# Optimization experiments

Measured on AMD Instinct MI355X. Metric: run time of the kernel, lower is better.

## Reference

```python
import jax, jax.numpy as jnp
import numpy as np

L, D, H, d = 16, 1024, 16, 64
NB, BS = 1024, 16        # num physical blocks, block size (tokens per block)
START_POS = 16368        # T = START_POS + L = 16384
SCALE = 1.0 / np.sqrt(d)


def setup_inputs() -> dict:
    key = jax.random.key(0)
    ks = jax.random.split(key, 5)
    return {
        "x": jax.random.normal(ks[0], (L, D), jnp.float32),
        "k_pool": jax.random.normal(ks[1], (NB, BS, H, d), jnp.float32),
        "v_pool": jax.random.normal(ks[2], (NB, BS, H, d), jnp.float32),
        "W_attn": jax.random.normal(ks[3], (D, 3 * D), jnp.float32) * 0.02,
        "b_attn": jnp.zeros((3 * D,), jnp.float32),
        "W_proj": jax.random.normal(ks[4], (D, D), jnp.float32) * 0.02,
        "b_proj": jnp.zeros((D,), jnp.float32),
        "block_ids": jnp.arange(NB, dtype=jnp.int64),
        "start_pos": START_POS,
    }


def reference(x, k_pool, v_pool, W_attn, b_attn, W_proj, b_proj, block_ids, start_pos):
    # QKV projection
    qkv = x @ W_attn + b_attn                      # [L, 3D]
    q, k, v = jnp.split(qkv, 3, axis=-1)
    q = q.reshape(L, H, d)
    k = k.reshape(L, H, d)
    v = v.reshape(L, H, d)

    # paged write of new K/V into the pool
    pos = start_pos + jnp.arange(L)                # logical positions of new tokens
    blk = block_ids[pos // BS]                     # physical block per token
    off = pos % BS
    k_pool = k_pool.at[blk, off].set(k)
    v_pool = v_pool.at[blk, off].set(v)

    # paged read of the full prefix [0, T)
    T = start_pos + L
    k_pos = jnp.arange(T)
    kb = block_ids[k_pos // BS]
    ko = k_pos % BS
    k_cache = k_pool[kb, ko]                       # [T, H, d]
    v_cache = v_pool[kb, ko]                       # [T, H, d]

    # attention: scores [H, L, T]
    scores = jnp.einsum("lhd,thd->hlt", q, k_cache) * SCALE
    mask = k_pos[None, :] > pos[:, None]           # [L, T] future positions
    scores = jnp.where(mask[None, :, :], -jnp.inf, scores)
    attn = jax.nn.softmax(scores.astype(jnp.float32), axis=-1).astype(scores.dtype)

    out = jnp.einsum("hlt,thd->lhd", attn, v_cache).reshape(L, D)
    return out @ W_proj + b_proj
```

## Files before the change

kernel.cpp:

```cpp
#include <hip/hip_runtime.h>
#include <math.h>

#define L_TOK 16
#define DMODEL 1024
#define NHEAD 16
#define DHEAD 64
#define NBLK 1024
#define BSZ 16
#define START_POS_C 16368
#define TTOT 16384
#define SPLITS 128
#define CHUNK 128
#define KSPLIT 16
#define QSCALE (0.125f * 1.4426950408889634f)

#define OFF_QKVP 0
#define OFF_QW   (OFF_QKVP + KSPLIT * L_TOK * 3 * DMODEL)
#define OFF_ACC  (OFF_QW + NHEAD * L_TOK * DHEAD)
#define OFF_M    (OFF_ACC + NHEAD * SPLITS * L_TOK * DHEAD)
#define OFF_SE   (OFF_M + NHEAD * SPLITS * L_TOK)
#define OFF_ATTN (OFF_SE + NHEAD * SPLITS * L_TOK)
#define OFF_PROJP (OFF_ATTN + L_TOK * DMODEL)

typedef _Float16 half4_t __attribute__((ext_vector_type(4)));
typedef _Float16 half8_t __attribute__((ext_vector_type(8)));
typedef float float4v __attribute__((ext_vector_type(4)));

union H8 { _Float16 h[8]; half8_t v; };
union H4 { _Float16 h[4]; half4_t v; };

#define GL4(dst, p, o) asm volatile("global_load_dwordx4 %0, %1, off offset:" #o : "=v"(dst) : "v"(p))
#define GL1(dst, p, o) asm volatile("global_load_dword %0, %1, off offset:" #o : "=v"(dst) : "v"(p))

__device__ __forceinline__ void load_batch(float* buf, const float* Wp, int bk, int ncols) {
#pragma unroll
    for (int i = 0; i < 16; ++i) buf[i] = Wp[(size_t)(bk + i) * ncols];
}

__device__ __forceinline__ void fma_batch(float4v* acc_, const float* buf,
                                          const float* sxT, int bk) {
#pragma unroll
    for (int i = 0; i < 16; ++i) {
        const float wv_ = buf[i];
        const float4v* xp = (const float4v*)&sxT[(bk + i) * 20];
        float4v xa = xp[0], xb = xp[1], xc = xp[2], xd = xp[3];
        acc_[0] += xa * wv_;
        acc_[1] += xb * wv_;
        acc_[2] += xc * wv_;
        acc_[3] += xd * wv_;
    }
}

__global__ __launch_bounds__(256) void gemm_part(const float* __restrict__ x,
                                                 const float* __restrict__ W,
                                                 float* __restrict__ part,
                                                 int ncols) {
    const int col = blockIdx.x * 256 + threadIdx.x;
    const int k0 = blockIdx.y * (DMODEL / KSPLIT);

    __shared__ __align__(16) float sxT[64 * 20];
#pragma unroll
    for (int i = threadIdx.x; i < 64 * 16; i += 256) {
        int k = i & 63, l = i >> 6;
        sxT[k * 20 + l] = x[(size_t)l * DMODEL + k0 + k];
    }

    const float* Wp = W + (size_t)k0 * ncols + col;
    float wa[16], wb[16];
    load_batch(wa, Wp, 0, ncols);
    load_batch(wb, Wp, 16, ncols);
    __builtin_amdgcn_sched_barrier(0);
    __syncthreads();

    float4v acc_[4];
#pragma unroll
    for (int g = 0; g < 4; ++g) acc_[g] = (float4v){0.f, 0.f, 0.f, 0.f};

    fma_batch(acc_, wa, sxT, 0);
    load_batch(wa, Wp, 32, ncols);
    __builtin_amdgcn_sched_barrier(0);
    fma_batch(acc_, wb, sxT, 16);
    load_batch(wb, Wp, 48, ncols);
    __builtin_amdgcn_sched_barrier(0);
    fma_batch(acc_, wa, sxT, 32);
    fma_batch(acc_, wb, sxT, 48);

    const size_t base = ((size_t)blockIdx.y * L_TOK) * ncols + col;
#pragma unroll
    for (int g = 0; g < 4; ++g)
#pragma unroll
        for (int j = 0; j < 4; ++j)
            part[base + (size_t)(4 * g + j) * ncols] = acc_[g][j];
}

__global__ __launch_bounds__(256) void qkv_reduce_scatter(const float* __restrict__ part,
                                                          const float* __restrict__ b_attn,
                                                          const int* __restrict__ block_ids,
                                                          float* __restrict__ qws,
                                                          float* __restrict__ kpool,
                                                          float* __restrict__ vpool) {
    int tid = blockIdx.x * 256 + threadIdx.x;
    int n = tid % (3 * DMODEL);
    int l = tid / (3 * DMODEL);
    float s = b_attn[n];
#pragma unroll
    for (int kb = 0; kb < KSPLIT; ++kb)
        s += part[((size_t)kb * L_TOK + l) * (3 * DMODEL) + n];
    int sec = n >> 10;
    int m = n & (DMODEL - 1);
    int h = m >> 6;
    int dd = m & 63;
    if (sec == 0) {
        qws[(h * L_TOK + l) * DHEAD + dd] = s * QSCALE;
    } else {
        int pos = START_POS_C + l;
        int blk = block_ids[pos >> 4];
        int off = pos & 15;
        size_t idx = (((size_t)blk * BSZ + off) * NHEAD + h) * DHEAD + dd;
        if (sec == 1) kpool[idx] = s;
        else          vpool[idx] = s;
    }
}

__global__ __launch_bounds__(256, 3) void paged_attn(const float* __restrict__ kpool,
                                                     const float* __restrict__ vpool,
                                                     const int* __restrict__ block_ids,
                                                     const float* __restrict__ qws,
                                                     float* __restrict__ accws,
                                                     float* __restrict__ m_arr,
                                                     float* __restrict__ se_arr) {
    const int h = blockIdx.x;
    const int s = blockIdx.y;
    const int tid = threadIdx.x;
    const int w = tid >> 6;
    const int lane = tid & 63;
    const int c = lane & 15;
    const int quad = lane >> 4;

    __shared__ __align__(16) float sacc[4][16][68];
    __shared__ float sm[4][16], sse[4][16];

    const int pb0 = block_ids[s * 8 + 2 * w];
    const int pb1 = block_ids[s * 8 + 2 * w + 1];
    const int tb0 = s * CHUNK + w * 32;
    const int tb1 = tb0 + 16;

    const float* qr  = qws + ((size_t)(h * L_TOK + c)) * DHEAD + quad * 8;
    const float* kr0 = kpool + (((size_t)pb0 * BSZ + c) * NHEAD + h) * DHEAD + quad * 8;
    const float* kr1 = kpool + (((size_t)pb1 * BSZ + c) * NHEAD + h) * DHEAD + quad * 8;
    const float* vb0 = vpool + ((size_t)pb0 * BSZ * NHEAD + h) * DHEAD + c;
    const float* vb1 = vpool + ((size_t)pb1 * BSZ * NHEAD + h) * DHEAD + c;

    float4v q0, q1, q2, q3, k0a, k0b, k0c, k0d, k1a, k1b, k1c, k1d;
    GL4(q0, qr, 0); GL4(q1, qr, 16); GL4(q2, qr, 128); GL4(q3, qr, 144);
    GL4(k0a, kr0, 0); GL4(k0b, kr0, 16); GL4(k0c, kr0, 128); GL4(k0d, kr0, 144);
    GL4(k1a, kr1, 0); GL4(k1b, kr1, 16); GL4(k1c, kr1, 128); GL4(k1d, kr1, 144);
    float v0_[4][4], v1_[4][4];
#pragma unroll
    for (int j = 0; j < 4; ++j) {
        const float* r0 = vb0 + (size_t)(4 * quad + j) * (NHEAD * DHEAD);
        GL1(v0_[j][0], r0, 0); GL1(v0_[j][1], r0, 64);
        GL1(v0_[j][2], r0, 128); GL1(v0_[j][3], r0, 192);
    }
#pragma unroll
    for (int j = 0; j < 4; ++j) {
        const float* r1 = vb1 + (size_t)(4 * quad + j) * (NHEAD * DHEAD);
        GL1(v1_[j][0], r1, 0); GL1(v1_[j][1], r1, 64);
        GL1(v1_[j][2], r1, 128); GL1(v1_[j][3], r1, 192);
    }
    asm volatile("s_waitcnt vmcnt(32)" ::: "memory");
    __builtin_amdgcn_sched_barrier(0);

    H8 qb0, qb1;
    qb0.h[0]=(_Float16)q0[0]; qb0.h[1]=(_Float16)q0[1]; qb0.h[2]=(_Float16)q0[2]; qb0.h[3]=(_Float16)q0[3];
    qb0.h[4]=(_Float16)q1[0]; qb0.h[5]=(_Float16)q1[1]; qb0.h[6]=(_Float16)q1[2]; qb0.h[7]=(_Float16)q1[3];
    qb1.h[0]=(_Float16)q2[0]; qb1.h[1]=(_Float16)q2[1]; qb1.h[2]=(_Float16)q2[2]; qb1.h[3]=(_Float16)q2[3];
    qb1.h[4]=(_Float16)q3[0]; qb1.h[5]=(_Float16)q3[1]; qb1.h[6]=(_Float16)q3[2]; qb1.h[7]=(_Float16)q3[3];

    const float4v z4 = {0.f, 0.f, 0.f, 0.f};
    H8 ka, kb;
    ka.h[0]=(_Float16)k0a[0]; ka.h[1]=(_Float16)k0a[1]; ka.h[2]=(_Float16)k0a[2]; ka.h[3]=(_Float16)k0a[3];
    ka.h[4]=(_Float16)k0b[0]; ka.h[5]=(_Float16)k0b[1]; ka.h[6]=(_Float16)k0b[2]; ka.h[7]=(_Float16)k0b[3];
    kb.h[0]=(_Float16)k0c[0]; kb.h[1]=(_Float16)k0c[1]; kb.h[2]=(_Float16)k0c[2]; kb.h[3]=(_Float16)k0c[3];
    kb.h[4]=(_Float16)k0d[0]; kb.h[5]=(_Float16)k0d[1]; kb.h[6]=(_Float16)k0d[2]; kb.h[7]=(_Float16)k0d[3];
    float4v st0 = __builtin_amdgcn_mfma_f32_16x16x32_f16(ka.v, qb0.v, z4, 0, 0, 0);
    st0 = __builtin_amdgcn_mfma_f32_16x16x32_f16(kb.v, qb1.v, st0, 0, 0, 0);
    ka.h[0]=(_Float16)k1a[0]; ka.h[1]=(_Float16)k1a[1]; ka.h[2]=(_Float16)k1a[2]; ka.h[3]=(_Float16)k1a[3];
    ka.h[4]=(_Float16)k1b[0]; ka.h[5]=(_Float16)k1b[1]; ka.h[6]=(_Float16)k1b[2]; ka.h[7]=(_Float16)k1b[3];
    kb.h[0]=(_Float16)k1c[0]; kb.h[1]=(_Float16)k1c[1]; kb.h[2]=(_Float16)k1c[2]; kb.h[3]=(_Float16)k1c[3];
    kb.h[4]=(_Float16)k1d[0]; kb.h[5]=(_Float16)k1d[1]; kb.h[6]=(_Float16)k1d[2]; kb.h[7]=(_Float16)k1d[3];
    float4v st1 = __builtin_amdgcn_mfma_f32_16x16x32_f16(ka.v, qb0.v, z4, 0, 0, 0);
    st1 = __builtin_amdgcn_mfma_f32_16x16x32_f16(kb.v, qb1.v, st1, 0, 0, 0);

    if (tb0 + 15 > START_POS_C) {
#pragma unroll
        for (int r = 0; r < 4; ++r)
            if (tb0 + 4 * quad + r > START_POS_C + c) st0[r] = -INFINITY;
    }
    if (tb1 + 15 > START_POS_C) {
#pragma unroll
        for (int r = 0; r < 4; ++r)
            if (tb1 + 4 * quad + r > START_POS_C + c) st1[r] = -INFINITY;
    }

    float tm = fmaxf(fmaxf(fmaxf(st0[0], st0[1]), fmaxf(st0[2], st0[3])),
                     fmaxf(fmaxf(st1[0], st1[1]), fmaxf(st1[2], st1[3])));
    tm = fmaxf(tm, __shfl_xor(tm, 16, 64));
    tm = fmaxf(tm, __shfl_xor(tm, 32, 64));
    H4 pa0, pa1;
    pa0.h[0]=(_Float16)exp2f(st0[0]-tm); pa0.h[1]=(_Float16)exp2f(st0[1]-tm);
    pa0.h[2]=(_Float16)exp2f(st0[2]-tm); pa0.h[3]=(_Float16)exp2f(st0[3]-tm);
    pa1.h[0]=(_Float16)exp2f(st1[0]-tm); pa1.h[1]=(_Float16)exp2f(st1[1]-tm);
    pa1.h[2]=(_Float16)exp2f(st1[2]-tm); pa1.h[3]=(_Float16)exp2f(st1[3]-tm);
    float ts = ((float)pa0.h[0] + (float)pa0.h[1]) + ((float)pa0.h[2] + (float)pa0.h[3])
             + ((float)pa1.h[0] + (float)pa1.h[1]) + ((float)pa1.h[2] + (float)pa1.h[3]);
    ts += __shfl_xor(ts, 16, 64);
    ts += __shfl_xor(ts, 32, 64);

    asm volatile("s_waitcnt vmcnt(0)" ::: "memory");
    __builtin_amdgcn_sched_barrier(0);

    float4v acc[4];
#pragma unroll
    for (int i = 0; i < 4; ++i) acc[i] = z4;
#pragma unroll
    for (int ndv = 0; ndv < 4; ++ndv) {
        H4 bf;
        bf.h[0]=(_Float16)v0_[0][ndv]; bf.h[1]=(_Float16)v0_[1][ndv];
        bf.h[2]=(_Float16)v0_[2][ndv]; bf.h[3]=(_Float16)v0_[3][ndv];
        acc[ndv] = __builtin_amdgcn_mfma_f32_16x16x16f16(pa0.v, bf.v, acc[ndv], 0, 0, 0);
        bf.h[0]=(_Float16)v1_[0][ndv]; bf.h[1]=(_Float16)v1_[1][ndv];
        bf.h[2]=(_Float16)v1_[2][ndv]; bf.h[3]=(_Float16)v1_[3][ndv];
        acc[ndv] = __builtin_amdgcn_mfma_f32_16x16x16f16(pa1.v, bf.v, acc[ndv], 0, 0, 0);
    }

#pragma unroll
    for (int ndv = 0; ndv < 4; ++ndv)
#pragma unroll
        for (int r = 0; r < 4; ++r)
            sacc[w][4 * quad + r][16 * ndv + c] = acc[ndv][r];
    if (quad == 0) { sm[w][c] = tm; sse[w][c] = ts; }
    __syncthreads();

    const int q = tid >> 4;
    const int dseg = tid & 15;
    float m0 = sm[0][q], m1 = sm[1][q], m2 = sm[2][q], m3 = sm[3][q];
    float M = fmaxf(fmaxf(m0, m1), fmaxf(m2, m3));
    float u0 = exp2f(m0 - M), u1 = exp2f(m1 - M), u2 = exp2f(m2 - M), u3 = exp2f(m3 - M);
    float den = u0 * sse[0][q] + u1 * sse[1][q] + u2 * sse[2][q] + u3 * sse[3][q];
    float4v num = u0 * (*(const float4v*)&sacc[0][q][4 * dseg])
                + u1 * (*(const float4v*)&sacc[1][q][4 * dseg])
                + u2 * (*(const float4v*)&sacc[2][q][4 * dseg])
                + u3 * (*(const float4v*)&sacc[3][q][4 * dseg]);
    const size_t ob = ((size_t)(h * SPLITS + s) * L_TOK + q) * DHEAD + 4 * dseg;
    *(float4v*)&accws[ob] = num;
    if (dseg == 0) {
        const size_t mb = (size_t)(h * SPLITS + s) * L_TOK + q;
        m_arr[mb] = M;
        se_arr[mb] = den;
    }
}

__global__ __launch_bounds__(256) void combine(const float* __restrict__ accws,
                                               const float* __restrict__ m_arr,
                                               const float* __restrict__ se_arr,
                                               float* __restrict__ attnws) {
    const int h = blockIdx.x >> 4;
    const int l = blockIdx.x & 15;
    const int w = threadIdx.x >> 6;
    const int lane = threadIdx.x & 63;
    __shared__ float sm[4], sse[4], sacc[4][64];

    const size_t base = (size_t)h * SPLITS * L_TOK + l;

    float mreg[SPLITS / 4];
#pragma unroll
    for (int i = 0; i < SPLITS / 4; ++i)
        mreg[i] = m_arr[base + (size_t)(w + 4 * i) * L_TOK];
    float M = -INFINITY;
#pragma unroll
    for (int i = 0; i < SPLITS / 4; ++i) M = fmaxf(M, mreg[i]);

    float num = 0.f, den = 0.f;
#pragma unroll
    for (int i = 0; i < SPLITS / 4; ++i) {
        const size_t idx = base + (size_t)(w + 4 * i) * L_TOK;
        const float wgt = exp2f(mreg[i] - M);
        num = fmaf(wgt, accws[idx * DHEAD + lane], num);
        den = fmaf(wgt, se_arr[idx], den);
    }

    if (lane == 0) { sm[w] = M; sse[w] = den; }
    sacc[w][lane] = num;
    __syncthreads();
    if (w == 0) {
        const float M0 = fmaxf(fmaxf(sm[0], sm[1]), fmaxf(sm[2], sm[3]));
        float nn = 0.f, dd = 0.f;
#pragma unroll
        for (int i = 0; i < 4; ++i) {
            const float wgt = exp2f(sm[i] - M0);
            nn = fmaf(wgt, sacc[i][lane], nn);
            dd = fmaf(wgt, sse[i], dd);
        }
        attnws[(size_t)l * DMODEL + h * DHEAD + lane] = nn / dd;
    }
}

__global__ __launch_bounds__(256) void proj_reduce(const float* __restrict__ part,
                                                   const float* __restrict__ bias,
                                                   float* __restrict__ out) {
    int tid = blockIdx.x * 256 + threadIdx.x;
    int n = tid & (DMODEL - 1);
    int l = tid >> 10;
    float s = bias[n];
#pragma unroll
    for (int kb = 0; kb < KSPLIT; ++kb)
        s += part[((size_t)kb * L_TOK + l) * DMODEL + n];
    out[tid] = s;
}

extern "C" void kernel_launch(void* const* d_in, const int* in_sizes, int n_in,
                              void* d_out, int out_size, void* d_ws, size_t ws_size,
                              hipStream_t stream) {
    const float* x       = (const float*)d_in[0];
    float* kpool         = (float*)d_in[1];
    float* vpool         = (float*)d_in[2];
    const float* W_attn  = (const float*)d_in[3];
    const float* b_attn  = (const float*)d_in[4];
    const float* W_proj  = (const float*)d_in[5];
    const float* b_proj  = (const float*)d_in[6];
    const int* block_ids = (const int*)d_in[7];
    float* ws  = (float*)d_ws;
    float* out = (float*)d_out;

    gemm_part<<<dim3(12, KSPLIT), 256, 0, stream>>>(x, W_attn, ws + OFF_QKVP, 3 * DMODEL);
    qkv_reduce_scatter<<<192, 256, 0, stream>>>(ws + OFF_QKVP, b_attn, block_ids,
                                                ws + OFF_QW, kpool, vpool);
    paged_attn<<<dim3(NHEAD, SPLITS), 256, 0, stream>>>(kpool, vpool, block_ids,
                                                        ws + OFF_QW, ws + OFF_ACC,
                                                        ws + OFF_M, ws + OFF_SE);
    combine<<<NHEAD * L_TOK, 256, 0, stream>>>(ws + OFF_ACC, ws + OFF_M, ws + OFF_SE,
                                               ws + OFF_ATTN);
    gemm_part<<<dim3(4, KSPLIT), 256, 0, stream>>>(ws + OFF_ATTN, W_proj, ws + OFF_PROJP, DMODEL);
    proj_reduce<<<64, 256, 0, stream>>>(ws + OFF_PROJP, b_proj, out);
}
```

Before: 195.7 us.

## Stage paged K/V through LDS via async global-to-LDS DMA with swizzle

The attention kernel now loads each warp's K and V paged blocks straight into shared memory with global_load_lds 16-byte DMA. It uses an XOR swizzle to avoid bank conflicts and reads MFMA operands from LDS, replacing the per-lane scalar V gathers and register-held K. This is meant to cut the number of memory instructions and the register pressure of scattered V loads. The trade is a 64KB LDS footprint, occupancy hint lowered from 3 to 2, and an added barrier. The split-K reduce kernels also load all partials first and then sum them as a tree, to expose memory-level parallelism.

```diff
diff --git a/kernel.cpp b/kernel.cpp
--- a/kernel.cpp
+++ b/kernel.cpp
@@ -29,8 +29,10 @@
 union H8 { _Float16 h[8]; half8_t v; };
 union H4 { _Float16 h[4]; half4_t v; };
 
-#define GL4(dst, p, o) asm volatile("global_load_dwordx4 %0, %1, off offset:" #o : "=v"(dst) : "v"(p))
-#define GL1(dst, p, o) asm volatile("global_load_dword %0, %1, off offset:" #o : "=v"(dst) : "v"(p))
+#define LDS_DMA16(gsrc, ldst)                                                        \
+    __builtin_amdgcn_global_load_lds(                                                \
+        (const __attribute__((address_space(1))) void*)(gsrc),                       \
+        (__attribute__((address_space(3))) void*)(ldst), 16, 0, 0)
 
 __device__ __forceinline__ void load_batch(float* buf, const float* Wp, int bk, int ncols) {
 #pragma unroll
@@ -102,10 +104,16 @@
     int tid = blockIdx.x * 256 + threadIdx.x;
     int n = tid % (3 * DMODEL);
     int l = tid / (3 * DMODEL);
+    float p[KSPLIT];
+#pragma unroll
+    for (int kb = 0; kb < KSPLIT; ++kb)
+        p[kb] = part[((size_t)kb * L_TOK + l) * (3 * DMODEL) + n];
     float s = b_attn[n];
 #pragma unroll
-    for (int kb = 0; kb < KSPLIT; ++kb)
-        s += part[((size_t)kb * L_TOK + l) * (3 * DMODEL) + n];
+    for (int st = 1; st < KSPLIT; st <<= 1)
+#pragma unroll
+        for (int i = 0; i < KSPLIT; i += 2 * st) p[i] += p[i + st];
+    s += p[0];
     int sec = n >> 10;
     int m = n & (DMODEL - 1);
     int h = m >> 6;
@@ -122,7 +130,7 @@
     }
 }
 
-__global__ __launch_bounds__(256, 3) void paged_attn(const float* __restrict__ kpool,
+__global__ __launch_bounds__(256, 2) void paged_attn(const float* __restrict__ kpool,
                                                      const float* __restrict__ vpool,
                                                      const int* __restrict__ block_ids,
                                                      const float* __restrict__ qws,
@@ -137,60 +145,87 @@
     const int c = lane & 15;
     const int quad = lane >> 4;
 
-    __shared__ __align__(16) float sacc[4][16][68];
+    __shared__ __align__(16) float smem[16384];
     __shared__ float sm[4][16], sse[4][16];
+    float* Klds = smem;
+    float* Vlds = smem + 8192;
+    float (*sacc)[16][68] = (float (*)[16][68])smem;
 
     const int pb0 = block_ids[s * 8 + 2 * w];
     const int pb1 = block_ids[s * 8 + 2 * w + 1];
     const int tb0 = s * CHUNK + w * 32;
     const int tb1 = tb0 + 16;
 
-    const float* qr  = qws + ((size_t)(h * L_TOK + c)) * DHEAD + quad * 8;
-    const float* kr0 = kpool + (((size_t)pb0 * BSZ + c) * NHEAD + h) * DHEAD + quad * 8;
-    const float* kr1 = kpool + (((size_t)pb1 * BSZ + c) * NHEAD + h) * DHEAD + quad * 8;
-    const float* vb0 = vpool + ((size_t)pb0 * BSZ * NHEAD + h) * DHEAD + c;
-    const float* vb1 = vpool + ((size_t)pb1 * BSZ * NHEAD + h) * DHEAD + c;
-
-    float4v q0, q1, q2, q3, k0a, k0b, k0c, k0d, k1a, k1b, k1c, k1d;
-    GL4(q0, qr, 0); GL4(q1, qr, 16); GL4(q2, qr, 128); GL4(q3, qr, 144);
-    GL4(k0a, kr0, 0); GL4(k0b, kr0, 16); GL4(k0c, kr0, 128); GL4(k0d, kr0, 144);
-    GL4(k1a, kr1, 0); GL4(k1b, kr1, 16); GL4(k1c, kr1, 128); GL4(k1d, kr1, 144);
-    float v0_[4][4], v1_[4][4];
-#pragma unroll
-    for (int j = 0; j < 4; ++j) {
-        const float* r0 = vb0 + (size_t)(4 * quad + j) * (NHEAD * DHEAD);
-        GL1(v0_[j][0], r0, 0); GL1(v0_[j][1], r0, 64);
-        GL1(v0_[j][2], r0, 128); GL1(v0_[j][3], r0, 192);
-    }
-#pragma unroll
-    for (int j = 0; j < 4; ++j) {
-        const float* r1 = vb1 + (size_t)(4 * quad + j) * (NHEAD * DHEAD);
-        GL1(v1_[j][0], r1, 0); GL1(v1_[j][1], r1, 64);
-        GL1(v1_[j][2], r1, 128); GL1(v1_[j][3], r1, 192);
-    }
-    asm volatile("s_waitcnt vmcnt(32)" ::: "memory");
+    const int off0 = quad * 4096 + (((c * 4) ^ (quad * 4)) * 4);
+    const int off4 = quad * 4096 + (((c * 4) ^ (quad * 4 + 16)) * 4);
+    const char* kg0 = (const char*)(kpool + ((size_t)pb0 * 256 + h) * 64);
+    const char* kg1 = (const char*)(kpool + ((size_t)pb1 * 256 + h) * 64);
+    const char* vg0 = (const char*)(vpool + ((size_t)pb0 * 256 + h) * 64);
+    const char* vg1 = (const char*)(vpool + ((size_t)pb1 * 256 + h) * 64);
+    float* kwb = Klds + (w * 32) * 64;
+    float* vwb = Vlds + (w * 32) * 64;
+
+    LDS_DMA16(kg0 + 0 * 4096 + off0, kwb + 0 * 64);
+    LDS_DMA16(kg0 + 4 * 4096 + off4, kwb + 4 * 64);
+    LDS_DMA16(kg0 + 8 * 4096 + off0, kwb + 8 * 64);
+    LDS_DMA16(kg0 + 12 * 4096 + off4, kwb + 12 * 64);
+    LDS_DMA16(kg1 + 0 * 4096 + off0, kwb + 16 * 64);
+    LDS_DMA16(kg1 + 4 * 4096 + off4, kwb + 20 * 64);
+    LDS_DMA16(kg1 + 8 * 4096 + off0, kwb + 24 * 64);
+    LDS_DMA16(kg1 + 12 * 4096 + off4, kwb + 28 * 64);
+    LDS_DMA16(vg0 + 0 * 4096 + off0, vwb + 0 * 64);
+    LDS_DMA16(vg0 + 4 * 4096 + off4, vwb + 4 * 64);
+    LDS_DMA16(vg0 + 8 * 4096 + off0, vwb + 8 * 64);
+    LDS_DMA16(vg0 + 12 * 4096 + off4, vwb + 12 * 64);
+    LDS_DMA16(vg1 + 0 * 4096 + off0, vwb + 16 * 64);
+    LDS_DMA16(vg1 + 4 * 4096 + off4, vwb + 20 * 64);
+    LDS_DMA16(vg1 + 8 * 4096 + off0, vwb + 24 * 64);
+    LDS_DMA16(vg1 + 12 * 4096 + off4, vwb + 28 * 64);
+
+    const float* qr = qws + ((size_t)(h * L_TOK + c)) * DHEAD + quad * 8;
+    float4 q0 = *(const float4*)(qr);
+    float4 q1 = *(const float4*)(qr + 4);
+    float4 q2 = *(const float4*)(qr + 32);
+    float4 q3 = *(const float4*)(qr + 36);
+
+    asm volatile("s_waitcnt vmcnt(0)" ::: "memory");
     __builtin_amdgcn_sched_barrier(0);
 
     H8 qb0, qb1;
-    qb0.h[0]=(_Float16)q0[0]; qb0.h[1]=(_Float16)q0[1]; qb0.h[2]=(_Float16)q0[2]; qb0.h[3]=(_Float16)q0[3];
-    qb0.h[4]=(_Float16)q1[0]; qb0.h[5]=(_Float16)q1[1]; qb0.h[6]=(_Float16)q1[2]; qb0.h[7]=(_Float16)q1[3];
-    qb1.h[0]=(_Float16)q2[0]; qb1.h[1]=(_Float16)q2[1]; qb1.h[2]=(_Float16)q2[2]; qb1.h[3]=(_Float16)q2[3];
-    qb1.h[4]=(_Float16)q3[0]; qb1.h[5]=(_Float16)q3[1]; qb1.h[6]=(_Float16)q3[2]; qb1.h[7]=(_Float16)q3[3];
-
+    qb0.h[0]=(_Float16)q0.x; qb0.h[1]=(_Float16)q0.y; qb0.h[2]=(_Float16)q0.z; qb0.h[3]=(_Float16)q0.w;
+    qb0.h[4]=(_Float16)q1.x; qb0.h[5]=(_Float16)q1.y; qb0.h[6]=(_Float16)q1.z; qb0.h[7]=(_Float16)q1.w;
+    qb1.h[0]=(_Float16)q2.x; qb1.h[1]=(_Float16)q2.y; qb1.h[2]=(_Float16)q2.z; qb1.h[3]=(_Float16)q2.w;
+    qb1.h[4]=(_Float16)q3.x; qb1.h[5]=(_Float16)q3.y; qb1.h[6]=(_Float16)q3.z; qb1.h[7]=(_Float16)q3.w;
+
+    const int sflt = (c & 7) * 4;
+    const float* krow0 = Klds + (size_t)(w * 32 + c) * 64;
+    const float* krow1 = krow0 + 16 * 64;
     const float4v z4 = {0.f, 0.f, 0.f, 0.f};
+
+    float4v kaa = *(const float4v*)&krow0[(quad * 8) ^ sflt];
+    float4v kab = *(const float4v*)&krow0[(quad * 8 + 4) ^ sflt];
+    float4v kac = *(const float4v*)&krow0[(32 + quad * 8) ^ sflt];
+    float4v kad = *(const float4v*)&krow0[(36 + quad * 8) ^ sflt];
     H8 ka, kb;
-    ka.h[0]=(_Float16)k0a[0]; ka.h[1]=(_Float16)k0a[1]; ka.h[2]=(_Float16)k0a[2]; ka.h[3]=(_Float16)k0a[3];
-    ka.h[4]=(_Float16)k0b[0]; ka.h[5]=(_Float16)k0b[1]; ka.h[6]=(_Float16)k0b[2]; ka.h[7]=(_Float16)k0b[3];
-    kb.h[0]=(_Float16)k0c[0]; kb.h[1]=(_Float16)k0c[1]; kb.h[2]=(_Float16)k0c[2]; kb.h[3]=(_Float16)k0c[3];
-    kb.h[4]=(_Float16)k0d[0]; kb.h[5]=(_Float16)k0d[1]; kb.h[6]=(_Float16)k0d[2]; kb.h[7]=(_Float16)k0d[3];
+    ka.h[0]=(_Float16)kaa[0]; ka.h[1]=(_Float16)kaa[1]; ka.h[2]=(_Float16)kaa[2]; ka.h[3]=(_Float16)kaa[3];
+    ka.h[4]=(_Float16)kab[0]; ka.h[5]=(_Float16)kab[1]; ka.h[6]=(_Float16)kab[2]; ka.h[7]=(_Float16)kab[3];
+    kb.h[0]=(_Float16)kac[0]; kb.h[1]=(_Float16)kac[1]; kb.h[2]=(_Float16)kac[2]; kb.h[3]=(_Float16)kac[3];
+    kb.h[4]=(_Float16)kad[0]; kb.h[5]=(_Float16)kad[1]; kb.h[6]=(_Float16)kad[2]; kb.h[7]=(_Float16)kad[3];
     float4v st0 = __builtin_amdgcn_mfma_f32_16x16x32_f16(ka.v, qb0.v, z4, 0, 0, 0);
     st0 = __builtin_amdgcn_mfma_f32_16x16x32_f16(kb.v, qb1.v, st0, 0, 0, 0);
-    ka.h[0]=(_Float16)k1a[0]; ka.h[1]=(_Float16)k1a[1]; ka.h[2]=(_Float16)k1a[2]; ka.h[3]=(_Float16)k1a[3];
-    ka.h[4]=(_Float16)k1b[0]; ka.h[5]=(_Float16)k1b[1]; ka.h[6]=(_Float16)k1b[2]; ka.h[7]=(_Float16)k1b[3];
-    kb.h[0]=(_Float16)k1c[0]; kb.h[1]=(_Float16)k1c[1]; kb.h[2]=(_Float16)k1c[2]; kb.h[3]=(_Float16)k1c[3];
-    kb.h[4]=(_Float16)k1d[0]; kb.h[5]=(_Float16)k1d[1]; kb.h[6]=(_Float16)k1d[2]; kb.h[7]=(_Float16)k1d[3];
+
+    kaa = *(const float4v*)&krow1[(quad * 8) ^ sflt];
+    kab = *(const float4v*)&krow1[(quad * 8 + 4) ^ sflt];
+    kac = *(const float4v*)&krow1[(32 + quad * 8) ^ sflt];
+    kad = *(const float4v*)&krow1[(36 + quad * 8) ^ sflt];
+    ka.h[0]=(_Float16)kaa[0]; ka.h[1]=(_Float16)kaa[1]; ka.h[2]=(_Float16)kaa[2]; ka.h[3]=(_Float16)kaa[3];
+    ka.h[4]=(_Float16)kab[0]; ka.h[5]=(_Float16)kab[1]; ka.h[6]=(_Float16)kab[2]; ka.h[7]=(_Float16)kab[3];
+    kb.h[0]=(_Float16)kac[0]; kb.h[1]=(_Float16)kac[1]; kb.h[2]=(_Float16)kac[2]; kb.h[3]=(_Float16)kac[3];
+    kb.h[4]=(_Float16)kad[0]; kb.h[5]=(_Float16)kad[1]; kb.h[6]=(_Float16)kad[2]; kb.h[7]=(_Float16)kad[3];
     float4v st1 = __builtin_amdgcn_mfma_f32_16x16x32_f16(ka.v, qb0.v, z4, 0, 0, 0);
     st1 = __builtin_amdgcn_mfma_f32_16x16x32_f16(kb.v, qb1.v, st1, 0, 0, 0);
+
+    __syncthreads();
 
     if (tb0 + 15 > START_POS_C) {
 #pragma unroll
@@ -217,20 +252,26 @@
     ts += __shfl_xor(ts, 16, 64);
     ts += __shfl_xor(ts, 32, 64);
 
-    asm volatile("s_waitcnt vmcnt(0)" ::: "memory");
-    __builtin_amdgcn_sched_barrier(0);
-
+    const float* vrb = Vlds + (size_t)(w * 32) * 64;
     float4v acc[4];
 #pragma unroll
     for (int i = 0; i < 4; ++i) acc[i] = z4;
 #pragma unroll
     for (int ndv = 0; ndv < 4; ++ndv) {
         H4 bf;
-        bf.h[0]=(_Float16)v0_[0][ndv]; bf.h[1]=(_Float16)v0_[1][ndv];
-        bf.h[2]=(_Float16)v0_[2][ndv]; bf.h[3]=(_Float16)v0_[3][ndv];
+#pragma unroll
+        for (int j = 0; j < 4; ++j) {
+            const int r = 4 * quad + j;
+            const int sw = (r & 7) * 4;
+            bf.h[j] = (_Float16)vrb[r * 64 + ((16 * ndv + c) ^ sw)];
+        }
         acc[ndv] = __builtin_amdgcn_mfma_f32_16x16x16f16(pa0.v, bf.v, acc[ndv], 0, 0, 0);
-        bf.h[0]=(_Float16)v1_[0][ndv]; bf.h[1]=(_Float16)v1_[1][ndv];
-        bf.h[2]=(_Float16)v1_[2][ndv]; bf.h[3]=(_Float16)v1_[3][ndv];
+#pragma unroll
+        for (int j = 0; j < 4; ++j) {
+            const int r = 4 * quad + j;
+            const int sw = (r & 7) * 4;
+            bf.h[j] = (_Float16)vrb[(16 + r) * 64 + ((16 * ndv + c) ^ sw)];
+        }
         acc[ndv] = __builtin_amdgcn_mfma_f32_16x16x16f16(pa1.v, bf.v, acc[ndv], 0, 0, 0);
     }
 
@@ -312,11 +353,15 @@
     int tid = blockIdx.x * 256 + threadIdx.x;
     int n = tid & (DMODEL - 1);
     int l = tid >> 10;
-    float s = bias[n];
+    float p[KSPLIT];
 #pragma unroll
     for (int kb = 0; kb < KSPLIT; ++kb)
-        s += part[((size_t)kb * L_TOK + l) * DMODEL + n];
-    out[tid] = s;
+        p[kb] = part[((size_t)kb * L_TOK + l) * DMODEL + n];
+#pragma unroll
+    for (int st = 1; st < KSPLIT; st <<= 1)
+#pragma unroll
+        for (int i = 0; i < KSPLIT; i += 2 * st) p[i] += p[i + st];
+    out[tid] = bias[n] + p[0];
 }
 
 extern "C" void kernel_launch(void* const* d_in, const int* in_sizes, int n_in,
```

Measured after the change: 194.0 us. Within noise of the previous version (-0.8%).

## Stage paged K/V tiles into LDS via async DMA with double buffering

Applied to the files above, without the earlier changes.

Rewrites paged_attn so each block handles 8 heads over a 128-token split. Whole 16-token K/V pool blocks are staged into swizzled LDS buffers with global_load_lds DMA, double-buffered across 8 iterations, and an online softmax runs per head. This replaces per-thread scattered dword V loads and the in-block cross-warp combine with contiguous 16-byte transfers overlapped with compute. The grid drops from 2048 to 256 blocks and uses 128KB of LDS at occupancy 1, which risks underfilling the GPU. The two reduce kernels also switch to tree-summing the split partials held in registers.

```diff
diff --git a/kernel.cpp b/kernel.cpp
--- a/kernel.cpp
+++ b/kernel.cpp
@@ -10,7 +10,6 @@
 #define START_POS_C 16368
 #define TTOT 16384
 #define SPLITS 128
-#define CHUNK 128
 #define KSPLIT 16
 #define QSCALE (0.125f * 1.4426950408889634f)
 
@@ -29,8 +28,10 @@
 union H8 { _Float16 h[8]; half8_t v; };
 union H4 { _Float16 h[4]; half4_t v; };
 
-#define GL4(dst, p, o) asm volatile("global_load_dwordx4 %0, %1, off offset:" #o : "=v"(dst) : "v"(p))
-#define GL1(dst, p, o) asm volatile("global_load_dword %0, %1, off offset:" #o : "=v"(dst) : "v"(p))
+#define LDS_DMA16(gsrc, ldst)                                                        \
+    __builtin_amdgcn_global_load_lds(                                                \
+        (const __attribute__((address_space(1))) void*)(gsrc),                       \
+        (__attribute__((address_space(3))) void*)(ldst), 16, 0, 0)
 
 __device__ __forceinline__ void load_batch(float* buf, const float* Wp, int bk, int ncols) {
 #pragma unroll
@@ -102,10 +103,16 @@
     int tid = blockIdx.x * 256 + threadIdx.x;
     int n = tid % (3 * DMODEL);
     int l = tid / (3 * DMODEL);
+    float p[KSPLIT];
+#pragma unroll
+    for (int kb = 0; kb < KSPLIT; ++kb)
+        p[kb] = part[((size_t)kb * L_TOK + l) * (3 * DMODEL) + n];
     float s = b_attn[n];
 #pragma unroll
-    for (int kb = 0; kb < KSPLIT; ++kb)
-        s += part[((size_t)kb * L_TOK + l) * (3 * DMODEL) + n];
+    for (int st = 1; st < KSPLIT; st <<= 1)
+#pragma unroll
+        for (int i = 0; i < KSPLIT; i += 2 * st) p[i] += p[i + st];
+    s += p[0];
     int sec = n >> 10;
     int m = n & (DMODEL - 1);
     int h = m >> 6;
@@ -122,14 +129,92 @@
     }
 }
 
-__global__ __launch_bounds__(256, 3) void paged_attn(const float* __restrict__ kpool,
+__device__ __forceinline__ void stage_tile(const float* __restrict__ kpool,
+                                           const float* __restrict__ vpool,
+                                           float* kb, float* vb, int blk,
+                                           int w, int lane, int hgrp) {
+    const float* gk = kpool + (size_t)blk * 16384;
+    const float* gv = vpool + (size_t)blk * 16384;
+#pragma unroll
+    for (int i = 0; i < 4; ++i) {
+        const int tok = 4 * w + i;
+        const int lx = lane ^ (tok & 7);
+#pragma unroll
+        for (int part = 0; part < 2; ++part) {
+            const size_t go = (size_t)tok * 1024 + hgrp * 512 + part * 256 + lx * 4;
+            LDS_DMA16(gk + go, kb + tok * 512 + part * 256);
+            LDS_DMA16(gv + go, vb + tok * 512 + part * 256);
+        }
+    }
+}
+
+__device__ __forceinline__ void attn_tile(const float* kt, const float* vt,
+                                          int hh, half8_t qlo, half8_t qhi,
+                                          float4v* acc, float& m_run, float& se_run,
+                                          int tb, int c, int quad) {
+    const int keyc = c & 7;
+    const int hb = hh << 4;
+    const float* krow = kt + c * 512;
+    float4v a0 = *(const float4v*)&krow[(((hb | (2 * quad)) ^ keyc) << 2)];
+    float4v a1 = *(const float4v*)&krow[(((hb | (2 * quad + 1)) ^ keyc) << 2)];
+    float4v a2 = *(const float4v*)&krow[(((hb | (2 * quad + 8)) ^ keyc) << 2)];
+    float4v a3 = *(const float4v*)&krow[(((hb | (2 * quad + 9)) ^ keyc) << 2)];
+    H8 ka, kb;
+    ka.h[0]=(_Float16)a0[0]; ka.h[1]=(_Float16)a0[1]; ka.h[2]=(_Float16)a0[2]; ka.h[3]=(_Float16)a0[3];
+    ka.h[4]=(_Float16)a1[0]; ka.h[5]=(_Float16)a1[1]; ka.h[6]=(_Float16)a1[2]; ka.h[7]=(_Float16)a1[3];
+    kb.h[0]=(_Float16)a2[0]; kb.h[1]=(_Float16)a2[1]; kb.h[2]=(_Float16)a2[2]; kb.h[3]=(_Float16)a2[3];
+    kb.h[4]=(_Float16)a3[0]; kb.h[5]=(_Float16)a3[1]; kb.h[6]=(_Float16)a3[2]; kb.h[7]=(_Float16)a3[3];
+    const float4v z4 = {0.f, 0.f, 0.f, 0.f};
+    float4v st = __builtin_amdgcn_mfma_f32_16x16x32_f16(ka.v, qlo, z4, 0, 0, 0);
+    st = __builtin_amdgcn_mfma_f32_16x16x32_f16(kb.v, qhi, st, 0, 0, 0);
+
+    if (tb + 15 > START_POS_C) {
+#pragma unroll
+        for (int r = 0; r < 4; ++r)
+            if (tb + 4 * quad + r > START_POS_C + c) st[r] = -INFINITY;
+    }
+
+    float tm = fmaxf(fmaxf(st[0], st[1]), fmaxf(st[2], st[3]));
+    tm = fmaxf(tm, __shfl_xor(tm, 16, 64));
+    tm = fmaxf(tm, __shfl_xor(tm, 32, 64));
+    const float m_new = fmaxf(m_run, tm);
+    const float fac = exp2f(m_run - m_new);
+    H4 pa;
+    pa.h[0]=(_Float16)exp2f(st[0]-m_new); pa.h[1]=(_Float16)exp2f(st[1]-m_new);
+    pa.h[2]=(_Float16)exp2f(st[2]-m_new); pa.h[3]=(_Float16)exp2f(st[3]-m_new);
+    float tsum = ((float)pa.h[0] + (float)pa.h[1]) + ((float)pa.h[2] + (float)pa.h[3]);
+    tsum += __shfl_xor(tsum, 16, 64);
+    tsum += __shfl_xor(tsum, 32, 64);
+    se_run = se_run * fac + tsum;
+    m_run = m_new;
+    float4v fv;
+    fv[0] = __shfl(fac, 4 * quad + 0, 64);
+    fv[1] = __shfl(fac, 4 * quad + 1, 64);
+    fv[2] = __shfl(fac, 4 * quad + 2, 64);
+    fv[3] = __shfl(fac, 4 * quad + 3, 64);
+#pragma unroll
+    for (int ndv = 0; ndv < 4; ++ndv) acc[ndv] *= fv;
+#pragma unroll
+    for (int ndv = 0; ndv < 4; ++ndv) {
+        H4 bf;
+#pragma unroll
+        for (int j = 0; j < 4; ++j) {
+            const int tokr = 4 * quad + j;
+            const int slot = (hb | (4 * ndv + (c >> 2))) ^ (tokr & 7);
+            bf.h[j] = (_Float16)vt[tokr * 512 + (slot << 2) + (c & 3)];
+        }
+        acc[ndv] = __builtin_amdgcn_mfma_f32_16x16x16f16(pa.v, bf.v, acc[ndv], 0, 0, 0);
+    }
+}
+
+__global__ __launch_bounds__(256, 1) void paged_attn(const float* __restrict__ kpool,
                                                      const float* __restrict__ vpool,
                                                      const int* __restrict__ block_ids,
                                                      const float* __restrict__ qws,
                                                      float* __restrict__ accws,
                                                      float* __restrict__ m_arr,
                                                      float* __restrict__ se_arr) {
-    const int h = blockIdx.x;
+    const int hgrp = blockIdx.x;
     const int s = blockIdx.y;
     const int tid = threadIdx.x;
     const int w = tid >> 6;
@@ -137,127 +222,77 @@
     const int c = lane & 15;
     const int quad = lane >> 4;
 
-    __shared__ __align__(16) float sacc[4][16][68];
-    __shared__ float sm[4][16], sse[4][16];
-
-    const int pb0 = block_ids[s * 8 + 2 * w];
-    const int pb1 = block_ids[s * 8 + 2 * w + 1];
-    const int tb0 = s * CHUNK + w * 32;
-    const int tb1 = tb0 + 16;
-
-    const float* qr  = qws + ((size_t)(h * L_TOK + c)) * DHEAD + quad * 8;
-    const float* kr0 = kpool + (((size_t)pb0 * BSZ + c) * NHEAD + h) * DHEAD + quad * 8;
-    const float* kr1 = kpool + (((size_t)pb1 * BSZ + c) * NHEAD + h) * DHEAD + quad * 8;
-    const float* vb0 = vpool + ((size_t)pb0 * BSZ * NHEAD + h) * DHEAD + c;
-    const float* vb1 = vpool + ((size_t)pb1 * BSZ * NHEAD + h) * DHEAD + c;
-
-    float4v q0, q1, q2, q3, k0a, k0b, k0c, k0d, k1a, k1b, k1c, k1d;
-    GL4(q0, qr, 0); GL4(q1, qr, 16); GL4(q2, qr, 128); GL4(q3, qr, 144);
-    GL4(k0a, kr0, 0); GL4(k0b, kr0, 16); GL4(k0c, kr0, 128); GL4(k0d, kr0, 144);
-    GL4(k1a, kr1, 0); GL4(k1b, kr1, 16); GL4(k1c, kr1, 128); GL4(k1d, kr1, 144);
-    float v0_[4][4], v1_[4][4];
-#pragma unroll
-    for (int j = 0; j < 4; ++j) {
-        const float* r0 = vb0 + (size_t)(4 * quad + j) * (NHEAD * DHEAD);
-        GL1(v0_[j][0], r0, 0); GL1(v0_[j][1], r0, 64);
-        GL1(v0_[j][2], r0, 128); GL1(v0_[j][3], r0, 192);
-    }
-#pragma unroll
-    for (int j = 0; j < 4; ++j) {
-        const float* r1 = vb1 + (size_t)(4 * quad + j) * (NHEAD * DHEAD);
-        GL1(v1_[j][0], r1, 0); GL1(v1_[j][1], r1, 64);
-        GL1(v1_[j][2], r1, 128); GL1(v1_[j][3], r1, 192);
-    }
-    asm volatile("s_waitcnt vmcnt(32)" ::: "memory");
-    __builtin_amdgcn_sched_barrier(0);
-
-    H8 qb0, qb1;
-    qb0.h[0]=(_Float16)q0[0]; qb0.h[1]=(_Float16)q0[1]; qb0.h[2]=(_Float16)q0[2]; qb0.h[3]=(_Float16)q0[3];
-    qb0.h[4]=(_Float16)q1[0]; qb0.h[5]=(_Float16)q1[1]; qb0.h[6]=(_Float16)q1[2]; qb0.h[7]=(_Float16)q1[3];
-    qb1.h[0]=(_Float16)q2[0]; qb1.h[1]=(_Float16)q2[1]; qb1.h[2]=(_Float16)q2[2]; qb1.h[3]=(_Float16)q2[3];
-    qb1.h[4]=(_Float16)q3[0]; qb1.h[5]=(_Float16)q3[1]; qb1.h[6]=(_Float16)q3[2]; qb1.h[7]=(_Float16)q3[3];
-
-    const float4v z4 = {0.f, 0.f, 0.f, 0.f};
-    H8 ka, kb;
-    ka.h[0]=(_Float16)k0a[0]; ka.h[1]=(_Float16)k0a[1]; ka.h[2]=(_Float16)k0a[2]; ka.h[3]=(_Float16)k0a[3];
-    ka.h[4]=(_Float16)k0b[0]; ka.h[5]=(_Float16)k0b[1]; ka.h[6]=(_Float16)k0b[2]; ka.h[7]=(_Float16)k0b[3];
-    kb.h[0]=(_Float16)k0c[0]; kb.h[1]=(_Float16)k0c[1]; kb.h[2]=(_Float16)k0c[2]; kb.h[3]=(_Float16)k0c[3];
-    kb.h[4]=(_Float16)k0d[0]; kb.h[5]=(_Float16)k0d[1]; kb.h[6]=(_Float16)k0d[2]; kb.h[7]=(_Float16)k0d[3];
-    float4v st0 = __builtin_amdgcn_mfma_f32_16x16x32_f16(ka.v, qb0.v, z4, 0, 0, 0);
-    st0 = __builtin_amdgcn_mfma_f32_16x16x32_f16(kb.v, qb1.v, st0, 0, 0, 0);
-    ka.h[0]=(_Float16)k1a[0]; ka.h[1]=(_Float16)k1a[1]; ka.h[2]=(_Float16)k1a[2]; ka.h[3]=(_Float16)k1a[3];
-    ka.h[4]=(_Float16)k1b[0]; ka.h[5]=(_Float16)k1b[1]; ka.h[6]=(_Float16)k1b[2]; ka.h[7]=(_Float16)k1b[3];
-    kb.h[0]=(_Float16)k1c[0]; kb.h[1]=(_Float16)k1c[1]; kb.h[2]=(_Float16)k1c[2]; kb.h[3]=(_Float16)k1c[3];
-    kb.h[4]=(_Float16)k1d[0]; kb.h[5]=(_Float16)k1d[1]; kb.h[6]=(_Float16)k1d[2]; kb.h[7]=(_Float16)k1d[3];
-    float4v st1 = __builtin_amdgcn_mfma_f32_16x16x32_f16(ka.v, qb0.v, z4, 0, 0, 0);
-    st1 = __builtin_amdgcn_mfma_f32_16x16x32_f16(kb.v, qb1.v, st1, 0, 0, 0);
-
-    if (tb0 + 15 > START_POS_C) {
-#pragma unroll
-        for (int r = 0; r < 4; ++r)
-            if (tb0 + 4 * quad + r > START_POS_C + c) st0[r] = -INFINITY;
-    }
-    if (tb1 + 15 > START_POS_C) {
-#pragma unroll
-        for (int r = 0; r < 4; ++r)
-            if (tb1 + 4 * quad + r > START_POS_C + c) st1[r] = -INFINITY;
-    }
-
-    float tm = fmaxf(fmaxf(fmaxf(st0[0], st0[1]), fmaxf(st0[2], st0[3])),
-                     fmaxf(fmaxf(st1[0], st1[1]), fmaxf(st1[2], st1[3])));
-    tm = fmaxf(tm, __shfl_xor(tm, 16, 64));
-    tm = fmaxf(tm, __shfl_xor(tm, 32, 64));
-    H4 pa0, pa1;
-    pa0.h[0]=(_Float16)exp2f(st0[0]-tm); pa0.h[1]=(_Float16)exp2f(st0[1]-tm);
-    pa0.h[2]=(_Float16)exp2f(st0[2]-tm); pa0.h[3]=(_Float16)exp2f(st0[3]-tm);
-    pa1.h[0]=(_Float16)exp2f(st1[0]-tm); pa1.h[1]=(_Float16)exp2f(st1[1]-tm);
-    pa1.h[2]=(_Float16)exp2f(st1[2]-tm); pa1.h[3]=(_Float16)exp2f(st1[3]-tm);
-    float ts = ((float)pa0.h[0] + (float)pa0.h[1]) + ((float)pa0.h[2] + (float)pa0.h[3])
-             + ((float)pa1.h[0] + (float)pa1.h[1]) + ((float)pa1.h[2] + (float)pa1.h[3]);
-    ts += __shfl_xor(ts, 16, 64);
-    ts += __shfl_xor(ts, 32, 64);
-
-    asm volatile("s_waitcnt vmcnt(0)" ::: "memory");
-    __builtin_amdgcn_sched_barrier(0);
-
-    float4v acc[4];
-#pragma unroll
-    for (int i = 0; i < 4; ++i) acc[i] = z4;
-#pragma unroll
-    for (int ndv = 0; ndv < 4; ++ndv) {
-        H4 bf;
-        bf.h[0]=(_Float16)v0_[0][ndv]; bf.h[1]=(_Float16)v0_[1][ndv];
-        bf.h[2]=(_Float16)v0_[2][ndv]; bf.h[3]=(_Float16)v0_[3][ndv];
-        acc[ndv] = __builtin_amdgcn_mfma_f32_16x16x16f16(pa0.v, bf.v, acc[ndv], 0, 0, 0);
-        bf.h[0]=(_Float16)v1_[0][ndv]; bf.h[1]=(_Float16)v1_[1][ndv];
-        bf.h[2]=(_Float16)v1_[2][ndv]; bf.h[3]=(_Float16)v1_[3][ndv];
-        acc[ndv] = __builtin_amdgcn_mfma_f32_16x16x16f16(pa1.v, bf.v, acc[ndv], 0, 0, 0);
-    }
-
+    __shared__ __align__(16) float kbuf[2][8192];
+    __shared__ __align__(16) float vbuf[2][8192];
+
+    int blks[8];
+#pragma unroll
+    for (int t = 0; t < 8; ++t) blks[t] = block_ids[s * 8 + t];
+
+    const int h0 = hgrp * 8 + 2 * w;
+    H8 qA0, qA1, qB0, qB1;
+    {
+        const float* qr = qws + ((size_t)(h0 * L_TOK + c)) * DHEAD + quad * 8;
+        float4 x0 = *(const float4*)(qr),        x1 = *(const float4*)(qr + 4);
+        float4 x2 = *(const float4*)(qr + 32),   x3 = *(const float4*)(qr + 36);
+        float4 y0 = *(const float4*)(qr + 1024), y1 = *(const float4*)(qr + 1028);
+        float4 y2 = *(const float4*)(qr + 1056), y3 = *(const float4*)(qr + 1060);
+        qA0.h[0]=(_Float16)x0.x; qA0.h[1]=(_Float16)x0.y; qA0.h[2]=(_Float16)x0.z; qA0.h[3]=(_Float16)x0.w;
+        qA0.h[4]=(_Float16)x1.x; qA0.h[5]=(_Float16)x1.y; qA0.h[6]=(_Float16)x1.z; qA0.h[7]=(_Float16)x1.w;
+        qA1.h[0]=(_Float16)x2.x; qA1.h[1]=(_Float16)x2.y; qA1.h[2]=(_Float16)x2.z; qA1.h[3]=(_Float16)x2.w;
+        qA1.h[4]=(_Float16)x3.x; qA1.h[5]=(_Float16)x3.y; qA1.h[6]=(_Float16)x3.z; qA1.h[7]=(_Float16)x3.w;
+        qB0.h[0]=(_Float16)y0.x; qB0.h[1]=(_Float16)y0.y; qB0.h[2]=(_Float16)y0.z; qB0.h[3]=(_Float16)y0.w;
+        qB0.h[4]=(_Float16)y1.x; qB0.h[5]=(_Float16)y1.y; qB0.h[6]=(_Float16)y1.z; qB0.h[7]=(_Float16)y1.w;
+        qB1.h[0]=(_Float16)y2.x; qB1.h[1]=(_Float16)y2.y; qB1.h[2]=(_Float16)y2.z; qB1.h[3]=(_Float16)y2.w;
+        qB1.h[4]=(_Float16)y3.x; qB1.h[5]=(_Float16)y3.y; qB1.h[6]=(_Float16)y3.z; qB1.h[7]=(_Float16)y3.w;
+    }
+
+    stage_tile(kpool, vpool, kbuf[0], vbuf[0], blks[0], w, lane, hgrp);
+
+    float4v accA[4], accB[4];
+#pragma unroll
+    for (int i = 0; i < 4; ++i) {
+        accA[i] = (float4v){0.f, 0.f, 0.f, 0.f};
+        accB[i] = (float4v){0.f, 0.f, 0.f, 0.f};
+    }
+    float mA = -INFINITY, seA = 0.f, mB = -INFINITY, seB = 0.f;
+
+    float* kc = kbuf[0]; float* vc = vbuf[0];
+    float* kn = kbuf[1]; float* vn = vbuf[1];
+
+    for (int t = 0; t < 8; ++t) {
+        if (t < 7) {
+            stage_tile(kpool, vpool, kn, vn, blks[t + 1], w, lane, hgrp);
+            asm volatile("s_waitcnt vmcnt(16)" ::: "memory");
+        } else {
+            asm volatile("s_waitcnt vmcnt(0)" ::: "memory");
+        }
+        __builtin_amdgcn_sched_barrier(0);
+        __builtin_amdgcn_s_barrier();
+
+        const int tb = s * 128 + t * 16;
+        attn_tile(kc, vc, 2 * w,     qA0.v, qA1.v, accA, mA, seA, tb, c, quad);
+        attn_tile(kc, vc, 2 * w + 1, qB0.v, qB1.v, accB, mB, seB, tb, c, quad);
+
+        __builtin_amdgcn_s_barrier();
+        float* tk = kc; kc = kn; kn = tk;
+        float* tv = vc; vc = vn; vn = tv;
+    }
+
+    const size_t obA = ((size_t)(h0 * SPLITS + s) * L_TOK) * DHEAD;
+    const size_t obB = ((size_t)((h0 + 1) * SPLITS + s) * L_TOK) * DHEAD;
 #pragma unroll
     for (int ndv = 0; ndv < 4; ++ndv)
 #pragma unroll
-        for (int r = 0; r < 4; ++r)
-            sacc[w][4 * quad + r][16 * ndv + c] = acc[ndv][r];
-    if (quad == 0) { sm[w][c] = tm; sse[w][c] = ts; }
-    __syncthreads();
-
-    const int q = tid >> 4;
-    const int dseg = tid & 15;
-    float m0 = sm[0][q], m1 = sm[1][q], m2 = sm[2][q], m3 = sm[3][q];
-    float M = fmaxf(fmaxf(m0, m1), fmaxf(m2, m3));
-    float u0 = exp2f(m0 - M), u1 = exp2f(m1 - M), u2 = exp2f(m2 - M), u3 = exp2f(m3 - M);
-    float den = u0 * sse[0][q] + u1 * sse[1][q] + u2 * sse[2][q] + u3 * sse[3][q];
-    float4v num = u0 * (*(const float4v*)&sacc[0][q][4 * dseg])
-                + u1 * (*(const float4v*)&sacc[1][q][4 * dseg])
-                + u2 * (*(const float4v*)&sacc[2][q][4 * dseg])
-                + u3 * (*(const float4v*)&sacc[3][q][4 * dseg]);
-    const size_t ob = ((size_t)(h * SPLITS + s) * L_TOK + q) * DHEAD + 4 * dseg;
-    *(float4v*)&accws[ob] = num;
-    if (dseg == 0) {
-        const size_t mb = (size_t)(h * SPLITS + s) * L_TOK + q;
-        m_arr[mb] = M;
-        se_arr[mb] = den;
+        for (int r = 0; r < 4; ++r) {
+            accws[obA + (size_t)(4 * quad + r) * DHEAD + 16 * ndv + c] = accA[ndv][r];
+            accws[obB + (size_t)(4 * quad + r) * DHEAD + 16 * ndv + c] = accB[ndv][r];
+        }
+    if (quad == 0) {
+        const size_t mbA = (size_t)(h0 * SPLITS + s) * L_TOK + c;
+        const size_t mbB = (size_t)((h0 + 1) * SPLITS + s) * L_TOK + c;
+        m_arr[mbA] = mA; se_arr[mbA] = seA;
+        m_arr[mbB] = mB; se_arr[mbB] = seB;
     }
 }
 
@@ -312,11 +347,15 @@
     int tid = blockIdx.x * 256 + threadIdx.x;
     int n = tid & (DMODEL - 1);
     int l = tid >> 10;
-    float s = bias[n];
+    float p[KSPLIT];
 #pragma unroll
     for (int kb = 0; kb < KSPLIT; ++kb)
-        s += part[((size_t)kb * L_TOK + l) * DMODEL + n];
-    out[tid] = s;
+        p[kb] = part[((size_t)kb * L_TOK + l) * DMODEL + n];
+#pragma unroll
+    for (int st = 1; st < KSPLIT; st <<= 1)
+#pragma unroll
+        for (int i = 0; i < KSPLIT; i += 2 * st) p[i] += p[i + st];
+    out[tid] = bias[n] + p[0];
 }
 
 extern "C" void kernel_launch(void* const* d_in, const int* in_sizes, int n_in,
@@ -336,9 +375,9 @@
     gemm_part<<<dim3(12, KSPLIT), 256, 0, stream>>>(x, W_attn, ws + OFF_QKVP, 3 * DMODEL);
     qkv_reduce_scatter<<<192, 256, 0, stream>>>(ws + OFF_QKVP, b_attn, block_ids,
                                                 ws + OFF_QW, kpool, vpool);
-    paged_attn<<<dim3(NHEAD, SPLITS), 256, 0, stream>>>(kpool, vpool, block_ids,
-                                                        ws + OFF_QW, ws + OFF_ACC,
-                                                        ws + OFF_M, ws + OFF_SE);
+    paged_attn<<<dim3(2, SPLITS), 256, 0, stream>>>(kpool, vpool, block_ids,
+                                                    ws + OFF_QW, ws + OFF_ACC,
+                                                    ws + OFF_M, ws + OFF_SE);
     combine<<<NHEAD * L_TOK, 256, 0, stream>>>(ws + OFF_ACC, ws + OFF_M, ws + OFF_SE,
                                                ws + OFF_ATTN);
     gemm_part<<<dim3(4, KSPLIT), 256, 0, stream>>>(ws + OFF_ATTN, W_proj, ws + OFF_PROJP, DMODEL);
```

Measured after the change: 196.9 us. About the same (+0.6%).
